# Kernel optimization log

Hardware: AMD Instinct MI355X
Metric: run time of the kernel (lower is better)

Reference implementation:

```python
import jax, jax.numpy as jnp
import numpy as np
from jax import lax

B, C, H, W = 8, 256, 128, 128
NH = 8
HD = C // NH
EPS = 1e-5


def setup_inputs() -> dict:
    key = jax.random.key(0)
    ks = jax.random.split(key, 6)
    x = jax.random.normal(ks[0], (B, C, H, W), dtype=jnp.float32)
    dw_weight = jax.random.normal(ks[1], (C, 1, 3, 3), dtype=jnp.float32) * 0.1
    off_weight = jax.random.normal(ks[2], (NH * 2, C), dtype=jnp.float32) * 0.05
    off_bias = jnp.zeros((NH * 2,), dtype=jnp.float32)
    v_weight = jax.random.normal(ks[3], (C, C), dtype=jnp.float32) * (1.0 / np.sqrt(C))
    o_weight = jax.random.normal(ks[4], (C, C), dtype=jnp.float32) * (1.0 / np.sqrt(C))
    gamma = jnp.ones((C,), dtype=jnp.float32)
    beta = jnp.zeros((C,), dtype=jnp.float32)
    return {"x": x, "dw_weight": dw_weight, "off_weight": off_weight, "off_bias": off_bias,
            "v_weight": v_weight, "o_weight": o_weight, "gamma": gamma, "beta": beta}


def reference(x, dw_weight, off_weight, off_bias, v_weight, o_weight, gamma, beta):
    b, c, h, w = x.shape
    # --- offset branch: depthwise 3x3 + pointwise 1x1 ---
    hdw = lax.conv_general_dilated(x, dw_weight, (1, 1), 'SAME',
                                   feature_group_count=c,
                                   dimension_numbers=('NCHW', 'OIHW', 'NCHW'))
    offsets = jnp.einsum('bchw,oc->bohw', hdw, off_weight) + off_bias[None, :, None, None]
    offsets = jnp.tanh(offsets) * 0.5                      # (B, 2*NH, H, W)
    offsets = offsets.reshape(b, NH, 2, h, w)
    dy, dx = offsets[:, :, 0], offsets[:, :, 1]            # (B, NH, H, W)

    # --- value projection, split into heads ---
    V = jnp.einsum('bchw,oc->bohw', x, v_weight).reshape(b, NH, HD, h, w)

    # --- deformable bilinear sampling (grid_sample, align_corners=True, border pad) ---
    gy = jnp.linspace(-1.0, 1.0, h, dtype=x.dtype)[None, None, :, None]
    gx = jnp.linspace(-1.0, 1.0, w, dtype=x.dtype)[None, None, None, :]
    sx = jnp.clip(gx + dx, -1.0, 1.0)                      # (B, NH, H, W)
    sy = jnp.clip(gy + dy, -1.0, 1.0)
    ix = (sx + 1.0) * 0.5 * (w - 1)                        # unnormalized coords
    iy = (sy + 1.0) * 0.5 * (h - 1)
    x0f = jnp.floor(ix); y0f = jnp.floor(iy)
    wx = ix - x0f; wy = iy - y0f
    x0 = jnp.clip(x0f.astype(jnp.int32), 0, w - 1)
    x1 = jnp.clip(x0f.astype(jnp.int32) + 1, 0, w - 1)
    y0 = jnp.clip(y0f.astype(jnp.int32), 0, h - 1)
    y1 = jnp.clip(y0f.astype(jnp.int32) + 1, 0, h - 1)

    Vf = V.reshape(b, NH, HD, h * w)

    def gather(yi, xi):
        idx = (yi * w + xi).reshape(b, NH, 1, h * w)
        return jnp.take_along_axis(Vf, idx, axis=3)        # (B, NH, HD, H*W)

    wx_ = wx.reshape(b, NH, 1, h * w); wy_ = wy.reshape(b, NH, 1, h * w)
    sampled = (gather(y0, x0) * (1 - wx_) * (1 - wy_)
               + gather(y0, x1) * wx_ * (1 - wy_)
               + gather(y1, x0) * (1 - wx_) * wy_
               + gather(y1, x1) * wx_ * wy_)
    out = sampled.reshape(b, c, h, w)

    # --- output projection + GroupNorm(NH groups) + residual ---
    out = jnp.einsum('bchw,oc->bohw', out, o_weight)
    g = out.reshape(b, NH, HD * h * w)
    mu = jnp.mean(g, axis=-1, keepdims=True)
    var = jnp.mean(jnp.square(g - mu), axis=-1, keepdims=True)
    g = (g - mu) * lax.rsqrt(var + EPS)
    out = g.reshape(b, c, h, w) * gamma[None, :, None, None] + beta[None, :, None, None]
    return x + out
```

## Files before the change

### kernel.cpp

```cpp
#include <hip/hip_runtime.h>
#include <hip/hip_bf16.h>

#define B_ 8
#define C_ 256
#define H_ 128
#define W_ 128
#define HW_ 16384
#define CHW_ (C_ * HW_)
#define NH_ 8
#define HD_ 32
#define NTOT (B_ * CHW_)

typedef short short8 __attribute__((ext_vector_type(8)));
typedef float f32x4 __attribute__((ext_vector_type(4)));

__global__ __launch_bounds__(256) void wconv_kernel(const float* __restrict__ vw,
                                                    const float* __restrict__ ow,
                                                    __hip_bfloat16* __restrict__ wvb,
                                                    __hip_bfloat16* __restrict__ wob) {
    int i = blockIdx.x * 256 + threadIdx.x;
    wvb[i] = __float2bfloat16(vw[i]);
    wob[i] = __float2bfloat16(ow[i]);
}

__global__ __launch_bounds__(256) void xt_kernel(const float* __restrict__ x,
                                                 __hip_bfloat16* __restrict__ xT) {
    __shared__ float tile[64][68];
    int t = threadIdx.x;
    int p0 = blockIdx.x * 64, c0 = blockIdx.y * 64, b = blockIdx.z;
    const float* xb = x + ((size_t)b * C_ + c0) * HW_ + p0;
#pragma unroll
    for (int l = 0; l < 4; ++l) {
        int idx = t + 256 * l;
        int row = idx >> 4, cf = idx & 15;
        float4 v = *(const float4*)&xb[(size_t)row * HW_ + cf * 4];
        *(float4*)&tile[row][cf * 4] = v;
    }
    __syncthreads();
    __hip_bfloat16* op = xT + ((size_t)b * HW_ + p0) * C_ + c0;
#pragma unroll
    for (int l = 0; l < 2; ++l) {
        int idx = t + 256 * l;
        int p = idx & 63, oct = idx >> 6;
        __hip_bfloat16 arr[8];
#pragma unroll
        for (int j = 0; j < 8; ++j) arr[j] = __float2bfloat16(tile[oct * 8 + j][p]);
        *(int4*)(op + (size_t)p * C_ + oct * 8) = *(int4*)arr;
    }
}

__global__ __launch_bounds__(256) void fused_offset_kernel(const float* __restrict__ x,
                                                           const float* __restrict__ dww,
                                                           const float* __restrict__ offw,
                                                           float* __restrict__ partials) {
    __shared__ float xt[4][10][136];
    __shared__ float wT[32][16];
    __shared__ float wd[32][9];
    int t = threadIdx.x;
    int rt = blockIdx.x, cg = blockIdx.y, b = blockIdx.z;
    int h0 = rt * 8, c0 = cg * 32;
    for (int i = t; i < 512; i += 256) { int o = i >> 5, c = i & 31; wT[c][o] = offw[o * 256 + c0 + c]; }
    for (int i = t; i < 288; i += 256) { wd[i / 9][i % 9] = dww[(c0 + i / 9) * 9 + i % 9]; }
    const float* xb = x + ((size_t)b * C_ + c0) * HW_;
    int col = t & 127;
    int sb = (t >> 7) * 4;
    float acc[4][16] = {};
    for (int cc0 = 0; cc0 < 32; cc0 += 4) {
        __syncthreads();
#pragma unroll
        for (int l = 0; l < 5; ++l) {
            int idx = t + 256 * l;
            int pr = idx >> 5, c4 = idx & 31;
            int cc = pr / 10, r = pr - cc * 10;
            int gh = h0 - 1 + r;
            float4 v = make_float4(0.f, 0.f, 0.f, 0.f);
            if (gh >= 0 && gh < H_)
                v = *(const float4*)&xb[(size_t)(cc0 + cc) * HW_ + gh * W_ + c4 * 4];
            *(float4*)&xt[cc][r][4 + c4 * 4] = v;
        }
        if (t < 80) { int pr = t >> 1, side = t & 1; xt[pr / 10][pr % 10][side ? 132 : 3] = 0.f; }
        __syncthreads();
#pragma unroll
        for (int cc = 0; cc < 4; ++cc) {
            float win[6][3];
#pragma unroll
            for (int rr = 0; rr < 6; ++rr)
#pragma unroll
                for (int kk = 0; kk < 3; ++kk)
                    win[rr][kk] = xt[cc][sb + rr][col + 3 + kk];
            float w9[9];
#pragma unroll
            for (int k9 = 0; k9 < 9; ++k9) w9[k9] = wd[cc0 + cc][k9];
#pragma unroll
            for (int j = 0; j < 4; ++j) {
                float s = 0.f;
#pragma unroll
                for (int ky = 0; ky < 3; ++ky)
#pragma unroll
                    for (int kx = 0; kx < 3; ++kx)
                        s += win[j + ky][kx] * w9[ky * 3 + kx];
#pragma unroll
                for (int o = 0; o < 16; ++o) acc[j][o] += s * wT[cc0 + cc][o];
            }
        }
    }
    float* pb = partials + (size_t)(cg * 8 + b) * 16 * HW_;
#pragma unroll
    for (int o = 0; o < 16; ++o)
#pragma unroll
        for (int j = 0; j < 4; ++j)
            pb[(size_t)o * HW_ + (h0 + sb + j) * W_ + col] = acc[j][o];
}

__global__ __launch_bounds__(256) void offreduce_kernel(const float* __restrict__ partials,
                                                        const float* __restrict__ offb,
                                                        float* __restrict__ off_buf) {
    int i = blockIdx.x * 256 + threadIdx.x;
    float s = 0.f;
#pragma unroll
    for (int cg = 0; cg < 8; ++cg) s += partials[(size_t)cg * 2097152 + i];
    int o = (i >> 14) & 15;
    off_buf[i] = tanhf(s + offb[o]) * 0.5f;
}

template<bool TRANS, bool STATS>
__global__ __launch_bounds__(256) void mfma_gemm(const __hip_bfloat16* __restrict__ Wb,
                                                 const __hip_bfloat16* __restrict__ Xt,
                                                 float* __restrict__ Y,
                                                 float* __restrict__ stats) {
    __shared__ __align__(16) short As[128][40];
    __shared__ __align__(16) short Bs[128][40];
    int t = threadIdx.x;
    int wave = t >> 6, lane = t & 63;
    int quad = lane >> 4, l16 = lane & 15;
    int b = blockIdx.z;
    int n0 = blockIdx.x * 128, m0 = blockIdx.y * 128;
    const short* Wp = (const short*)Wb + (size_t)m0 * 256;
    const short* Xp = (const short*)Xt + ((size_t)b * HW_ + n0) * 256;
    int sr = t >> 2, sq = t & 3;
    f32x4 acc[2][8];
#pragma unroll
    for (int mt = 0; mt < 2; ++mt)
#pragma unroll
        for (int nt = 0; nt < 8; ++nt) acc[mt][nt] = (f32x4){0.f, 0.f, 0.f, 0.f};
    for (int k0 = 0; k0 < 256; k0 += 32) {
        int4 a0 = *(const int4*)(Wp + (size_t)sr * 256 + k0 + sq * 8);
        int4 a1 = *(const int4*)(Wp + (size_t)(sr + 64) * 256 + k0 + sq * 8);
        int4 b0 = *(const int4*)(Xp + (size_t)sr * 256 + k0 + sq * 8);
        int4 b1 = *(const int4*)(Xp + (size_t)(sr + 64) * 256 + k0 + sq * 8);
        __syncthreads();
        *(int4*)&As[sr][sq * 8] = a0;
        *(int4*)&As[sr + 64][sq * 8] = a1;
        *(int4*)&Bs[sr][sq * 8] = b0;
        *(int4*)&Bs[sr + 64][sq * 8] = b1;
        __syncthreads();
        short8 af[2], bf[8];
#pragma unroll
        for (int mt = 0; mt < 2; ++mt)
            af[mt] = *(const short8*)&As[wave * 32 + mt * 16 + l16][quad * 8];
#pragma unroll
        for (int nt = 0; nt < 8; ++nt)
            bf[nt] = *(const short8*)&Bs[nt * 16 + l16][quad * 8];
#pragma unroll
        for (int mt = 0; mt < 2; ++mt)
#pragma unroll
            for (int nt = 0; nt < 8; ++nt)
                acc[mt][nt] = __builtin_amdgcn_mfma_f32_16x16x32_bf16(af[mt], bf[nt], acc[mt][nt], 0, 0, 0);
    }
    float* Yb = Y + (size_t)b * CHW_;
    if constexpr (TRANS) {
#pragma unroll
        for (int mt = 0; mt < 2; ++mt)
#pragma unroll
            for (int nt = 0; nt < 8; ++nt) {
                int m = m0 + wave * 32 + mt * 16 + quad * 4;
                int n = n0 + nt * 16 + l16;
                *(f32x4*)&Yb[(size_t)n * C_ + m] = acc[mt][nt];
            }
    } else {
#pragma unroll
        for (int mt = 0; mt < 2; ++mt)
#pragma unroll
            for (int nt = 0; nt < 8; ++nt)
#pragma unroll
                for (int r = 0; r < 4; ++r) {
                    int m = m0 + wave * 32 + mt * 16 + quad * 4 + r;
                    int n = n0 + nt * 16 + l16;
                    Yb[(size_t)m * HW_ + n] = acc[mt][nt][r];
                }
    }
    if constexpr (STATS) {
        float s1 = 0.f, s2 = 0.f;
#pragma unroll
        for (int mt = 0; mt < 2; ++mt)
#pragma unroll
            for (int nt = 0; nt < 8; ++nt)
#pragma unroll
                for (int r = 0; r < 4; ++r) {
                    float v = acc[mt][nt][r];
                    s1 += v;
                    s2 += v * v;
                }
#pragma unroll
        for (int o = 32; o; o >>= 1) {
            s1 += __shfl_down(s1, o);
            s2 += __shfl_down(s2, o);
        }
        if (lane == 0) {
            int grp = b * NH_ + (m0 >> 5) + wave;
            atomicAdd(&stats[grp * 2 + 0], s1);
            atomicAdd(&stats[grp * 2 + 1], s2);
        }
    }
}

__global__ __launch_bounds__(256) void sample_kernel(const float* __restrict__ VT,
                                                     const float* __restrict__ off,
                                                     __hip_bfloat16* __restrict__ sT) {
    int t = threadIdx.x;
    int chunk = t & 7;
    int g = t >> 3;
    int head = g & 7;
    int p = blockIdx.x * 4 + (g >> 3);
    int b = blockIdx.z;
    int h = p >> 7, w = p & 127;
    const float* ob = off + ((size_t)b * 16 + head * 2) * HW_ + p;
    float dy = ob[0], dx = ob[HW_];
    float gy = h * (2.0f / 127.0f) - 1.0f;
    float gx = w * (2.0f / 127.0f) - 1.0f;
    float sx = fminf(fmaxf(gx + dx, -1.0f), 1.0f);
    float sy = fminf(fmaxf(gy + dy, -1.0f), 1.0f);
    float ix = (sx + 1.0f) * 0.5f * 127.0f;
    float iy = (sy + 1.0f) * 0.5f * 127.0f;
    float x0f = floorf(ix), y0f = floorf(iy);
    float wx = ix - x0f, wy = iy - y0f;
    int x0 = min(max((int)x0f, 0), 127);
    int x1 = min((int)x0f + 1, 127);
    int y0 = min(max((int)y0f, 0), 127);
    int y1 = min((int)y0f + 1, 127);
    float w00 = (1.f - wx) * (1.f - wy), w01 = wx * (1.f - wy);
    float w10 = (1.f - wx) * wy, w11 = wx * wy;
    const float* Vb = VT + (size_t)b * CHW_ + head * 32 + chunk * 4;
    float4 v00 = *(const float4*)(Vb + (size_t)(y0 * W_ + x0) * C_);
    float4 v01 = *(const float4*)(Vb + (size_t)(y0 * W_ + x1) * C_);
    float4 v10 = *(const float4*)(Vb + (size_t)(y1 * W_ + x0) * C_);
    float4 v11 = *(const float4*)(Vb + (size_t)(y1 * W_ + x1) * C_);
    __hip_bfloat16 arr[4];
    arr[0] = __float2bfloat16(v00.x * w00 + v01.x * w01 + v10.x * w10 + v11.x * w11);
    arr[1] = __float2bfloat16(v00.y * w00 + v01.y * w01 + v10.y * w10 + v11.y * w11);
    arr[2] = __float2bfloat16(v00.z * w00 + v01.z * w01 + v10.z * w10 + v11.z * w11);
    arr[3] = __float2bfloat16(v00.w * w00 + v01.w * w01 + v10.w * w10 + v11.w * w11);
    __hip_bfloat16* op = sT + ((size_t)b * HW_ + p) * C_ + head * 32 + chunk * 4;
    *(int2*)op = *(int2*)arr;
}

__global__ __launch_bounds__(256) void final_kernel(const float* __restrict__ x,
                                                    const float* __restrict__ stats,
                                                    const float* __restrict__ gamma,
                                                    const float* __restrict__ beta,
                                                    float* __restrict__ out) {
    int idx = (blockIdx.x * 256 + threadIdx.x) * 4;
    int c = (idx >> 14) & 255;
    int b = idx >> 22;
    int grp = b * NH_ + (c >> 5);
    const float invN = 1.0f / (float)(HD_ * HW_);
    float mu = stats[grp * 2 + 0] * invN;
    float var = stats[grp * 2 + 1] * invN - mu * mu;
    float r = rsqrtf(var + 1e-5f);
    float g = gamma[c], be = beta[c];
    float4 v = *(const float4*)&out[idx];
    float4 xv = *(const float4*)&x[idx];
    float4 o;
    o.x = xv.x + (v.x - mu) * r * g + be;
    o.y = xv.y + (v.y - mu) * r * g + be;
    o.z = xv.z + (v.z - mu) * r * g + be;
    o.w = xv.w + (v.w - mu) * r * g + be;
    *(float4*)&out[idx] = o;
}

extern "C" void kernel_launch(void* const* d_in, const int* in_sizes, int n_in,
                              void* d_out, int out_size, void* d_ws, size_t ws_size,
                              hipStream_t stream) {
    const float* x     = (const float*)d_in[0];
    const float* dww   = (const float*)d_in[1];
    const float* offw  = (const float*)d_in[2];
    const float* offb  = (const float*)d_in[3];
    const float* vw    = (const float*)d_in[4];
    const float* ow    = (const float*)d_in[5];
    const float* gamma = (const float*)d_in[6];
    const float* beta  = (const float*)d_in[7];
    float* out = (float*)d_out;
    float* ws_f = (float*)d_ws;

    float* partials = ws_f;
    float* off_buf  = ws_f + 16777216;
    float* stats    = ws_f + 18874368;
    __hip_bfloat16* wvb = (__hip_bfloat16*)(ws_f + 18874624);
    __hip_bfloat16* wob = wvb + 65536;
    __hip_bfloat16* xT  = (__hip_bfloat16*)(ws_f + 18940160);
    __hip_bfloat16* sT  = (__hip_bfloat16*)partials;

    wconv_kernel<<<256, 256, 0, stream>>>(vw, ow, wvb, wob);
    xt_kernel<<<dim3(256, 4, 8), 256, 0, stream>>>(x, xT);
    fused_offset_kernel<<<dim3(16, 8, 8), 256, 0, stream>>>(x, dww, offw, partials);
    offreduce_kernel<<<8192, 256, 0, stream>>>(partials, offb, off_buf);
    mfma_gemm<true, false><<<dim3(128, 2, 8), 256, 0, stream>>>(wvb, xT, out, nullptr);
    sample_kernel<<<dim3(4096, 1, 8), 256, 0, stream>>>(out, off_buf, sT);
    hipMemsetAsync(stats, 0, 128 * sizeof(float), stream);
    mfma_gemm<false, true><<<dim3(128, 2, 8), 256, 0, stream>>>(wob, sT, out, stats);
    final_kernel<<<NTOT / 1024, 256, 0, stream>>>(x, stats, gamma, beta, out);
}
```

Measured before the change: 593.8 us.

## Store V in bf16, stage full-K B tile in swizzled LDS, preload A fragments

The value-projection GEMM now writes V transposed as bf16 instead of fp32, halving the intermediate traffic. The sampling kernel gathers 8 bf16 channels per thread with 16-byte loads and uses half as many blocks. The GEMM loads the whole 128x256 B tile into XOR-swizzled LDS once and keeps A fragments in registers straight from global memory, which removes the per-k-step double syncthreads. The cost is 64KB of LDS per block, which lowers occupancy, and bf16 rounding of V before the bilinear interpolation.

```diff
diff --git a/kernel.cpp b/kernel.cpp
--- a/kernel.cpp
+++ b/kernel.cpp
@@ -126,10 +126,9 @@
 template<bool TRANS, bool STATS>
 __global__ __launch_bounds__(256) void mfma_gemm(const __hip_bfloat16* __restrict__ Wb,
                                                  const __hip_bfloat16* __restrict__ Xt,
-                                                 float* __restrict__ Y,
+                                                 void* __restrict__ Y,
                                                  float* __restrict__ stats) {
-    __shared__ __align__(16) short As[128][40];
-    __shared__ __align__(16) short Bs[128][40];
+    __shared__ __align__(16) short Bs[128 * 256];
     int t = threadIdx.x;
     int wave = t >> 6, lane = t & 63;
     int quad = lane >> 4, l16 = lane & 15;
@@ -137,47 +136,74 @@
     int n0 = blockIdx.x * 128, m0 = blockIdx.y * 128;
     const short* Wp = (const short*)Wb + (size_t)m0 * 256;
     const short* Xp = (const short*)Xt + ((size_t)b * HW_ + n0) * 256;
-    int sr = t >> 2, sq = t & 3;
+
+    int s = lane & 31;
+    int rbase = wave * 32 + (lane >> 5);
+#pragma unroll
+    for (int half = 0; half < 2; ++half) {
+        int4 st[8];
+#pragma unroll
+        for (int i = 0; i < 8; ++i) {
+            int n = rbase + half * 16 + i * 2;
+            st[i] = *(const int4*)(Xp + (size_t)n * 256 + s * 8);
+        }
+#pragma unroll
+        for (int i = 0; i < 8; ++i) {
+            int n = rbase + half * 16 + i * 2;
+            int sw = (s & 24) | ((s ^ n) & 7);
+            *(int4*)((char*)Bs + n * 512 + sw * 16) = st[i];
+        }
+    }
+
+    short8 af[8][2];
+#pragma unroll
+    for (int ks = 0; ks < 8; ++ks)
+#pragma unroll
+        for (int mt = 0; mt < 2; ++mt) {
+            int m = wave * 32 + mt * 16 + l16;
+            af[ks][mt] = *(const short8*)(Wp + (size_t)m * 256 + ks * 32 + quad * 8);
+        }
+
     f32x4 acc[2][8];
 #pragma unroll
     for (int mt = 0; mt < 2; ++mt)
 #pragma unroll
         for (int nt = 0; nt < 8; ++nt) acc[mt][nt] = (f32x4){0.f, 0.f, 0.f, 0.f};
-    for (int k0 = 0; k0 < 256; k0 += 32) {
-        int4 a0 = *(const int4*)(Wp + (size_t)sr * 256 + k0 + sq * 8);
-        int4 a1 = *(const int4*)(Wp + (size_t)(sr + 64) * 256 + k0 + sq * 8);
-        int4 b0 = *(const int4*)(Xp + (size_t)sr * 256 + k0 + sq * 8);
-        int4 b1 = *(const int4*)(Xp + (size_t)(sr + 64) * 256 + k0 + sq * 8);
-        __syncthreads();
-        *(int4*)&As[sr][sq * 8] = a0;
-        *(int4*)&As[sr + 64][sq * 8] = a1;
-        *(int4*)&Bs[sr][sq * 8] = b0;
-        *(int4*)&Bs[sr + 64][sq * 8] = b1;
-        __syncthreads();
-        short8 af[2], bf[8];
+
+    __syncthreads();
+
+#pragma unroll
+    for (int ks = 0; ks < 8; ++ks) {
+        short8 bf[8];
+#pragma unroll
+        for (int nt = 0; nt < 8; ++nt) {
+            int n = nt * 16 + l16;
+            int slot = ks * 4 + quad;
+            int sw = (slot & 24) | ((slot ^ n) & 7);
+            bf[nt] = *(const short8*)((const char*)Bs + n * 512 + sw * 16);
+        }
 #pragma unroll
         for (int mt = 0; mt < 2; ++mt)
-            af[mt] = *(const short8*)&As[wave * 32 + mt * 16 + l16][quad * 8];
-#pragma unroll
-        for (int nt = 0; nt < 8; ++nt)
-            bf[nt] = *(const short8*)&Bs[nt * 16 + l16][quad * 8];
-#pragma unroll
-        for (int mt = 0; mt < 2; ++mt)
 #pragma unroll
             for (int nt = 0; nt < 8; ++nt)
-                acc[mt][nt] = __builtin_amdgcn_mfma_f32_16x16x32_bf16(af[mt], bf[nt], acc[mt][nt], 0, 0, 0);
-    }
-    float* Yb = Y + (size_t)b * CHW_;
+                acc[mt][nt] = __builtin_amdgcn_mfma_f32_16x16x32_bf16(af[ks][mt], bf[nt], acc[mt][nt], 0, 0, 0);
+    }
+
     if constexpr (TRANS) {
+        __hip_bfloat16* Yb = (__hip_bfloat16*)Y + (size_t)b * CHW_;
 #pragma unroll
         for (int mt = 0; mt < 2; ++mt)
 #pragma unroll
             for (int nt = 0; nt < 8; ++nt) {
                 int m = m0 + wave * 32 + mt * 16 + quad * 4;
                 int n = n0 + nt * 16 + l16;
-                *(f32x4*)&Yb[(size_t)n * C_ + m] = acc[mt][nt];
+                __hip_bfloat16 arr[4];
+#pragma unroll
+                for (int r = 0; r < 4; ++r) arr[r] = __float2bfloat16(acc[mt][nt][r]);
+                *(int2*)((__hip_bfloat16*)Yb + (size_t)n * C_ + m) = *(int2*)arr;
             }
     } else {
+        float* Yb = (float*)Y + (size_t)b * CHW_;
 #pragma unroll
         for (int mt = 0; mt < 2; ++mt)
 #pragma unroll
@@ -214,14 +240,14 @@
     }
 }
 
-__global__ __launch_bounds__(256) void sample_kernel(const float* __restrict__ VT,
+__global__ __launch_bounds__(256) void sample_kernel(const __hip_bfloat16* __restrict__ VT,
                                                      const float* __restrict__ off,
                                                      __hip_bfloat16* __restrict__ sT) {
     int t = threadIdx.x;
-    int chunk = t & 7;
-    int g = t >> 3;
+    int chunk = t & 3;
+    int g = t >> 2;
     int head = g & 7;
-    int p = blockIdx.x * 4 + (g >> 3);
+    int p = blockIdx.x * 8 + (g >> 3);
     int b = blockIdx.z;
     int h = p >> 7, w = p & 127;
     const float* ob = off + ((size_t)b * 16 + head * 2) * HW_ + p;
@@ -240,18 +266,22 @@
     int y1 = min((int)y0f + 1, 127);
     float w00 = (1.f - wx) * (1.f - wy), w01 = wx * (1.f - wy);
     float w10 = (1.f - wx) * wy, w11 = wx * wy;
-    const float* Vb = VT + (size_t)b * CHW_ + head * 32 + chunk * 4;
-    float4 v00 = *(const float4*)(Vb + (size_t)(y0 * W_ + x0) * C_);
-    float4 v01 = *(const float4*)(Vb + (size_t)(y0 * W_ + x1) * C_);
-    float4 v10 = *(const float4*)(Vb + (size_t)(y1 * W_ + x0) * C_);
-    float4 v11 = *(const float4*)(Vb + (size_t)(y1 * W_ + x1) * C_);
-    __hip_bfloat16 arr[4];
-    arr[0] = __float2bfloat16(v00.x * w00 + v01.x * w01 + v10.x * w10 + v11.x * w11);
-    arr[1] = __float2bfloat16(v00.y * w00 + v01.y * w01 + v10.y * w10 + v11.y * w11);
-    arr[2] = __float2bfloat16(v00.z * w00 + v01.z * w01 + v10.z * w10 + v11.z * w11);
-    arr[3] = __float2bfloat16(v00.w * w00 + v01.w * w01 + v10.w * w10 + v11.w * w11);
-    __hip_bfloat16* op = sT + ((size_t)b * HW_ + p) * C_ + head * 32 + chunk * 4;
-    *(int2*)op = *(int2*)arr;
+    const short* Vb = (const short*)VT + (size_t)b * CHW_ + head * 32 + chunk * 8;
+    short8 v00 = *(const short8*)(Vb + (size_t)(y0 * W_ + x0) * C_);
+    short8 v01 = *(const short8*)(Vb + (size_t)(y0 * W_ + x1) * C_);
+    short8 v10 = *(const short8*)(Vb + (size_t)(y1 * W_ + x0) * C_);
+    short8 v11 = *(const short8*)(Vb + (size_t)(y1 * W_ + x1) * C_);
+    __hip_bfloat16 arr[8];
+#pragma unroll
+    for (int j = 0; j < 8; ++j) {
+        float f = __bfloat162float(((const __hip_bfloat16*)&v00)[j]) * w00 +
+                  __bfloat162float(((const __hip_bfloat16*)&v01)[j]) * w01 +
+                  __bfloat162float(((const __hip_bfloat16*)&v10)[j]) * w10 +
+                  __bfloat162float(((const __hip_bfloat16*)&v11)[j]) * w11;
+        arr[j] = __float2bfloat16(f);
+    }
+    __hip_bfloat16* op = sT + ((size_t)b * HW_ + p) * C_ + head * 32 + chunk * 8;
+    *(int4*)op = *(int4*)arr;
 }
 
 __global__ __launch_bounds__(256) void final_kernel(const float* __restrict__ x,
@@ -299,14 +329,15 @@
     __hip_bfloat16* wob = wvb + 65536;
     __hip_bfloat16* xT  = (__hip_bfloat16*)(ws_f + 18940160);
     __hip_bfloat16* sT  = (__hip_bfloat16*)partials;
+    __hip_bfloat16* vT  = (__hip_bfloat16*)out;
 
     wconv_kernel<<<256, 256, 0, stream>>>(vw, ow, wvb, wob);
     xt_kernel<<<dim3(256, 4, 8), 256, 0, stream>>>(x, xT);
     fused_offset_kernel<<<dim3(16, 8, 8), 256, 0, stream>>>(x, dww, offw, partials);
     offreduce_kernel<<<8192, 256, 0, stream>>>(partials, offb, off_buf);
-    mfma_gemm<true, false><<<dim3(128, 2, 8), 256, 0, stream>>>(wvb, xT, out, nullptr);
-    sample_kernel<<<dim3(4096, 1, 8), 256, 0, stream>>>(out, off_buf, sT);
+    mfma_gemm<true, false><<<dim3(128, 2, 8), 256, 0, stream>>>(wvb, xT, (void*)vT, nullptr);
+    sample_kernel<<<dim3(2048, 1, 8), 256, 0, stream>>>(vT, off_buf, sT);
     hipMemsetAsync(stats, 0, 128 * sizeof(float), stream);
-    mfma_gemm<false, true><<<dim3(128, 2, 8), 256, 0, stream>>>(wob, sT, out, stats);
+    mfma_gemm<false, true><<<dim3(128, 2, 8), 256, 0, stream>>>(wob, sT, (void*)out, stats);
     final_kernel<<<NTOT / 1024, 256, 0, stream>>>(x, stats, gamma, beta, out);
 }
```

Measured after the change: 566.1 us. 1.05x faster.
